# Kernel tuning notes

Hardware: AMD Instinct MI355X
Metric: run time of the kernel (lower is better)

The kernel has to match this reference:

```python
import jax, jax.numpy as jnp
import numpy as np

B, L, D = 4, 2048, 2048
H, KVH, HD = 16, 4, 128          # num_heads, num_kv_heads, head_dim = D // H
M = 16                           # mem_tokens
BASE = 10000.0
EPS = 1.1920929e-07              # torch F.rms_norm default eps = fp32 machine eps


def _rms_norm(x):
    # normalize over last dim, no learned weight (matches F.rms_norm(x, (hd,)))
    return x * jax.lax.rsqrt(jnp.mean(x * x, axis=-1, keepdims=True) + EPS)


def _apply_rotary(x, cos, sin):
    # x: [B, h, T, HD]; cos/sin: [1, 1, T, HD//2]
    half = x.shape[-1] // 2
    x1, x2 = x[..., :half], x[..., half:]
    return jnp.concatenate([x1 * cos + x2 * sin, -x1 * sin + x2 * cos], axis=-1)


def setup_inputs() -> dict:
    key = jax.random.key(0)
    k0, k1, k2, k3, k4 = jax.random.split(key, 5)
    kv_dim = KVH * HD
    s = 0.02
    return {
        "x": jax.random.normal(k0, (B, L, D), dtype=jnp.float32),
        "Wq": jax.random.normal(k1, (D, D), dtype=jnp.float32) * s,
        "Wk": jax.random.normal(k2, (kv_dim, D), dtype=jnp.float32) * s,
        "Wv": jax.random.normal(k3, (kv_dim, D), dtype=jnp.float32) * s,
        "Wproj": jax.random.normal(k4, (D, D), dtype=jnp.float32) * s,
        "q_gain": jnp.full((H,), 1.0, dtype=jnp.float32),
    }


def reference(x, Wq, Wk, Wv, Wproj, q_gain):
    Bx, Lx, Dx = x.shape
    # QKV projections (Linear: x @ W.T), split into heads -> [B, h, L, HD]
    q = (x @ Wq.T).reshape(Bx, Lx, H, HD).transpose(0, 2, 1, 3)
    k = (x @ Wk.T).reshape(Bx, Lx, KVH, HD).transpose(0, 2, 1, 3)
    v = (x @ Wv.T).reshape(Bx, Lx, KVH, HD).transpose(0, 2, 1, 3)
    # QK RMSNorm
    q = _rms_norm(q)
    k = _rms_norm(k)
    # RoPE on the non-memory tokens only
    T = Lx - M
    inv_freq = 1.0 / BASE ** (jnp.arange(0, HD, 2, dtype=jnp.float32) / HD)
    freqs = jnp.outer(jnp.arange(T, dtype=jnp.float32), inv_freq)  # [T, HD//2]
    cos = jnp.cos(freqs)[None, None]
    sin = jnp.sin(freqs)[None, None]
    q = jnp.concatenate([q[:, :, :M], _apply_rotary(q[:, :, M:], cos, sin)], axis=2)
    k = jnp.concatenate([k[:, :, :M], _apply_rotary(k[:, :, M:], cos, sin)], axis=2)
    # per-head gain on q
    q = q * q_gain[None, :, None, None]
    # GQA attention: group q heads by kv head (matches repeat_interleave ordering)
    rep = H // KVH
    qg = q.reshape(Bx, KVH, rep, Lx, HD)
    scale = 1.0 / np.sqrt(HD).astype(np.float32)
    scores = jnp.einsum('bgrqd,bgkd->bgrqk', qg, k) * scale  # [B, KVH, rep, L, L]
    causal = jnp.tril(jnp.ones((Lx, Lx), dtype=bool))
    scores = jnp.where(causal, scores, -jnp.inf)
    p = jax.nn.softmax(scores, axis=-1)
    y = jnp.einsum('bgrqk,bgkd->bgrqd', p, v)                # [B, KVH, rep, L, HD]
    y = y.reshape(Bx, H, Lx, HD).transpose(0, 2, 1, 3).reshape(Bx, Lx, Dx)
    return y @ Wproj.T
```

## Files before the change

### kernel.cpp

```cpp
#include <hip/hip_runtime.h>
#include <stdint.h>

typedef unsigned short u16;
typedef short s8v __attribute__((ext_vector_type(8)));
typedef float f4v __attribute__((ext_vector_type(4)));
typedef float f16v __attribute__((ext_vector_type(16)));

typedef __attribute__((address_space(1))) char gchar;
typedef __attribute__((address_space(3))) char lchar;

static __device__ __forceinline__ u16 f2bf(float f) {
  uint32_t x = __float_as_uint(f);
  x += 0x7fffu + ((x >> 16) & 1u);
  return (u16)(x >> 16);
}
static __device__ __forceinline__ float bf2f(u16 u) {
  return __uint_as_float(((uint32_t)u) << 16);
}
static __device__ __forceinline__ void gload_lds16(const void* g, void* l) {
  __builtin_amdgcn_global_load_lds((gchar*)(uintptr_t)g,
                                   (lchar*)(uint32_t)(uintptr_t)l, 16, 0, 0);
}

__global__ __launch_bounds__(256) void prep(const float4* __restrict__ x,
                                            const float4* __restrict__ wq,
                                            const float4* __restrict__ wk,
                                            const float4* __restrict__ wv,
                                            const float4* __restrict__ wp,
                                            uint2* __restrict__ xbf,
                                            uint2* __restrict__ wbf,
                                            float* __restrict__ tc,
                                            float* __restrict__ ts) {
  const int gid = blockIdx.x * 256 + threadIdx.x;
  const int st = gridDim.x * 256;
  for (int i = gid; i < 4194304; i += st) {
    float4 v = x[i];
    uint2 o;
    o.x = (uint32_t)f2bf(v.x) | ((uint32_t)f2bf(v.y) << 16);
    o.y = (uint32_t)f2bf(v.z) | ((uint32_t)f2bf(v.w) << 16);
    xbf[i] = o;
  }
  for (int i = gid; i < 2621440; i += st) {
    const float4* s;
    int off;
    if (i < 1048576)      { s = wq; off = i; }
    else if (i < 1310720) { s = wk; off = i - 1048576; }
    else if (i < 1572864) { s = wv; off = i - 1310720; }
    else                  { s = wp; off = i - 1572864; }
    float4 v = s[off];
    uint2 o;
    o.x = (uint32_t)f2bf(v.x) | ((uint32_t)f2bf(v.y) << 16);
    o.y = (uint32_t)f2bf(v.z) | ((uint32_t)f2bf(v.w) << 16);
    wbf[i] = o;
  }
  for (int i = gid; i < 2032 * 64; i += st) {
    int t = i >> 6, f = i & 63;
    float invf = 1.0f / powf(10000.0f, (float)f * (1.0f / 64.0f));
    float ang = (float)t * invf;
    float s, c;
    sincosf(ang, &s, &c);
    tc[i] = c;
    ts[i] = s;
  }
}

template <int OUT>
static __device__ __forceinline__ void gemm8_body(
    u16* sm, int bid, const u16* __restrict__ A, const u16* __restrict__ Wt,
    u16* __restrict__ Oa, float* __restrict__ OF) {
  const int tid = threadIdx.x;
  const int lane = tid & 63, wid = tid >> 6;
  const int wr = wid >> 2, wc = wid & 3;
  const int l15 = lane & 15, l4 = lane >> 4;

  const int swz = (bid & 7) * 32 + (bid >> 3);
  const int bm = swz >> 3, bn = swz & 7;
  const int m0 = bm * 256;
  const int n0r = bn * 256;

  auto pA = [&](int bs, int ks) { return sm + (bs * 2 + ks) * 8192; };
  auto pB = [&](int bs, int ks) { return sm + 32768 + (bs * 2 + ks) * 8192; };

  auto stage_part = [&](int kt, int bs, int ks) {
    const int kb = kt * 64 + ks * 32;
#pragma unroll
    for (int c = 0; c < 2; ++c) {
      int cidx = tid + c * 512;
      int r = cidx >> 2, q = cidx & 3;
      int cc = q ^ ((r >> 2) & 3);
      gload_lds16(A + (size_t)(m0 + r) * 2048 + kb + cc * 8,
                  pA(bs, ks) + cidx * 8);
    }
#pragma unroll
    for (int c = 0; c < 2; ++c) {
      int cidx = tid + c * 512;
      int r = cidx >> 2, q = cidx & 3;
      int cc = q ^ ((r >> 2) & 3);
      gload_lds16(Wt + (size_t)(n0r + r) * 2048 + kb + cc * 8,
                  pB(bs, ks) + cidx * 8);
    }
  };
  auto roff = [&](int fr, int c) {
    return (fr * 4 + (c ^ ((fr >> 2) & 3))) * 8;
  };

  const f4v Z4 = {0.f, 0.f, 0.f, 0.f};
  f4v acc[8][4];
#pragma unroll
  for (int i = 0; i < 8; i++)
#pragma unroll
    for (int j = 0; j < 4; j++) acc[i][j] = Z4;

  stage_part(0, 0, 0); stage_part(0, 0, 1);
  stage_part(1, 1, 0); stage_part(1, 1, 1);

  const int NT = 32;
  for (int t = 0; t < NT; ++t) {
    const int bs = t & 1;
    if (t + 1 < NT) asm volatile("s_waitcnt vmcnt(8)" ::: "memory");
    else            asm volatile("s_waitcnt vmcnt(0)" ::: "memory");
    asm volatile("s_barrier" ::: "memory");
    const bool pf = (t + 2 < NT);
#pragma unroll
    for (int ks = 0; ks < 2; ++ks) {
      s8v a[8], b[4];
#pragma unroll
      for (int i = 0; i < 8; ++i)
        a[i] = *(const s8v*)&pA(bs, ks)[roff(wr * 128 + i * 16 + l15, l4)];
#pragma unroll
      for (int j = 0; j < 4; ++j)
        b[j] = *(const s8v*)&pB(bs, ks)[roff(wc * 64 + j * 16 + l15, l4)];
      asm volatile("s_waitcnt lgkmcnt(0)" ::: "memory");
      __builtin_amdgcn_sched_barrier(0);
      asm volatile("s_barrier" ::: "memory");
      if (pf) stage_part(t + 2, bs, ks);
      __builtin_amdgcn_s_setprio(1);
#pragma unroll
      for (int i = 0; i < 8; ++i)
#pragma unroll
        for (int j = 0; j < 4; ++j)
          acc[i][j] = __builtin_amdgcn_mfma_f32_16x16x32_bf16(a[i], b[j], acc[i][j], 0, 0, 0);
      __builtin_amdgcn_s_setprio(0);
    }
  }

  const int colg = bn * 256 + wc * 64;
  if constexpr (OUT == 0) {
    const int hh = colg >> 7, d0 = colg & 127;
#pragma unroll
    for (int i = 0; i < 8; i++)
#pragma unroll
      for (int r = 0; r < 4; r++) {
        int m = m0 + wr * 128 + i * 16 + l4 * 4 + r;
        int b2 = m >> 11, l = m & 2047;
        size_t base = ((size_t)(b2 * 16 + hh) * 2048 + l) * 128 + d0;
#pragma unroll
        for (int j = 0; j < 4; j++)
          Oa[base + j * 16 + l15] = f2bf(acc[i][j][r]);
      }
  } else {
#pragma unroll
    for (int i = 0; i < 8; i++)
#pragma unroll
      for (int r = 0; r < 4; r++) {
        int m = m0 + wr * 128 + i * 16 + l4 * 4 + r;
#pragma unroll
        for (int j = 0; j < 4; j++)
          OF[(size_t)m * 2048 + colg + j * 16 + l15] = acc[i][j][r];
      }
  }
}

static __device__ __forceinline__ void gemm_kv_body(
    u16* sm, int bid, const u16* __restrict__ A, const u16* __restrict__ Wt,
    u16* __restrict__ Oa, u16* __restrict__ Ob2) {
  constexpr int MI = 4;
  const int tid = threadIdx.x;
  const int lane = tid & 63, wid = tid >> 6;
  const int wr = wid >> 1, wc = wid & 1;
  const int l15 = lane & 15, l4 = lane >> 4;

  const int swz = (bid & 7) * 32 + (bid >> 3);
  const int bm = swz >> 3, bn = swz & 7;
  const int m0 = bm * 256;
  const int n0r = bn * 128;

  auto pA = [&](int bs, int ks) { return sm + (bs * 2 + ks) * 8192; };
  auto pB = [&](int bs, int ks) { return sm + 32768 + (bs * 2 + ks) * 4096; };

  auto stage_part = [&](int kt, int bs, int ks) {
    const int kb = kt * 64 + ks * 32;
#pragma unroll
    for (int c = 0; c < 2; ++c) {
      int cidx = tid + c * 512;
      int r = cidx >> 2, q = cidx & 3;
      int cc = q ^ ((r >> 2) & 3);
      gload_lds16(A + (size_t)(m0 + r) * 2048 + kb + cc * 8,
                  pA(bs, ks) + cidx * 8);
    }
    {
      int cidx = tid;
      int r = cidx >> 2, q = cidx & 3;
      int cc = q ^ ((r >> 2) & 3);
      gload_lds16(Wt + (size_t)(n0r + r) * 2048 + kb + cc * 8,
                  pB(bs, ks) + cidx * 8);
    }
  };
  auto roff = [&](int fr, int c) {
    return (fr * 4 + (c ^ ((fr >> 2) & 3))) * 8;
  };

  const f4v Z4 = {0.f, 0.f, 0.f, 0.f};
  f4v acc[MI][4];
#pragma unroll
  for (int i = 0; i < MI; i++)
#pragma unroll
    for (int j = 0; j < 4; j++) acc[i][j] = Z4;

  stage_part(0, 0, 0); stage_part(0, 0, 1);
  stage_part(1, 1, 0); stage_part(1, 1, 1);

  const int NT = 32;
  for (int t = 0; t < NT; ++t) {
    const int bs = t & 1;
    if (t + 1 < NT) asm volatile("s_waitcnt vmcnt(6)" ::: "memory");
    else            asm volatile("s_waitcnt vmcnt(0)" ::: "memory");
    asm volatile("s_barrier" ::: "memory");
    const bool pf = (t + 2 < NT);
#pragma unroll
    for (int ks = 0; ks < 2; ++ks) {
      s8v afrg[MI], bfrg[4];
#pragma unroll
      for (int i = 0; i < MI; ++i)
        afrg[i] = *(const s8v*)&pA(bs, ks)[roff(wr * (MI * 16) + i * 16 + l15, l4)];
#pragma unroll
      for (int j = 0; j < 4; ++j)
        bfrg[j] = *(const s8v*)&pB(bs, ks)[roff(wc * 64 + j * 16 + l15, l4)];
      asm volatile("s_waitcnt lgkmcnt(0)" ::: "memory");
      __builtin_amdgcn_sched_barrier(0);
      asm volatile("s_barrier" ::: "memory");
      if (pf) stage_part(t + 2, bs, ks);
      __builtin_amdgcn_s_setprio(1);
#pragma unroll
      for (int i = 0; i < MI; ++i)
#pragma unroll
        for (int j = 0; j < 4; ++j)
          acc[i][j] = __builtin_amdgcn_mfma_f32_16x16x32_bf16(afrg[i], bfrg[j], acc[i][j], 0, 0, 0);
      __builtin_amdgcn_s_setprio(0);
    }
  }

  const int colg = bn * 128 + wc * 64;
  u16* Ob = (colg < 512) ? Oa : Ob2;
  const int hh = (colg & 511) >> 7, d0 = colg & 127;
#pragma unroll
  for (int i = 0; i < MI; i++)
#pragma unroll
    for (int r = 0; r < 4; r++) {
      int m = m0 + wr * (MI * 16) + i * 16 + l4 * 4 + r;
      int b = m >> 11, l = m & 2047;
      size_t base = ((size_t)(b * 4 + hh) * 2048 + l) * 128 + d0;
#pragma unroll
      for (int j = 0; j < 4; j++)
        Ob[base + j * 16 + l15] = f2bf(acc[i][j][r]);
    }
}

__global__ __launch_bounds__(512, 2) void gemm_qkv(
    const u16* __restrict__ x, const u16* __restrict__ wq,
    const u16* __restrict__ wkv, u16* __restrict__ q,
    u16* __restrict__ kO, u16* __restrict__ vO) {
  __shared__ u16 smem[65536];
  const int bid = (int)blockIdx.x;
  if (bid < 256) gemm8_body<0>(smem, bid, x, wq, q, nullptr);
  else           gemm_kv_body(smem, bid - 256, x, wkv, kO, vO);
}

__global__ __launch_bounds__(512, 2) void gemm_proj(
    const u16* __restrict__ y, const u16* __restrict__ wp, float* __restrict__ out) {
  __shared__ u16 smem[65536];
  gemm8_body<2>(smem, (int)blockIdx.x, y, wp, nullptr, out);
}

__global__ __launch_bounds__(256) void norm_transpose(
    u16* __restrict__ kbuf, const u16* __restrict__ v, u16* __restrict__ vt,
    const float* __restrict__ tc, const float* __restrict__ ts) {
  __shared__ u16 t[64][64];
  const int bid = (int)blockIdx.x;
  const int tid = threadIdx.x;
  if (bid < 1024) {
    const int l0 = (bid & 31) * 64, d0 = ((bid >> 5) & 1) * 64, bg = bid >> 6;
#pragma unroll
    for (int it = 0; it < 2; ++it) {
      int lin = it * 256 + tid;
      int r = lin >> 3, cb = lin & 7;
      s8v val = *(const s8v*)&v[((bg * 2048 + l0 + r) * 128) + d0 + cb * 8];
      *(s8v*)&t[r][(cb ^ (r & 7)) * 8] = val;
    }
    __syncthreads();
#pragma unroll
    for (int it = 0; it < 2; ++it) {
      int lin = it * 256 + tid;
      int r2 = lin >> 3, c2 = (lin & 7) * 8;
      s8v o;
#pragma unroll
      for (int j = 0; j < 8; ++j) {
        int rr = c2 + j, cc = r2;
        o[j] = (short)t[rr][(cc & 7) + 8 * ((cc >> 3) ^ (rr & 7))];
      }
      *(s8v*)&vt[((bg * 128 + d0 + r2) * 2048) + l0 + c2] = o;
    }
  } else {
    const int lane = tid & 63;
    const int gw = (bid - 1024) * 4 + (tid >> 6);
    for (int row = gw; row < 32768; row += 1024) {
      int l = row & 2047;
      u16* p = kbuf + (size_t)row * 128;
      float x1 = bf2f(p[lane]);
      float x2 = bf2f(p[lane + 64]);
      float ss = x1 * x1 + x2 * x2;
#pragma unroll
      for (int off = 32; off > 0; off >>= 1) ss += __shfl_xor(ss, off, 64);
      float r = rsqrtf(ss * (1.0f / 128.0f) + 1.1920929e-07f);
      x1 *= r; x2 *= r;
      if (l >= 16) {
        int tt = l - 16;
        float c = tc[tt * 64 + lane], s = ts[tt * 64 + lane];
        float o1 = x1 * c + x2 * s;
        float o2 = -x1 * s + x2 * c;
        x1 = o1; x2 = o2;
      }
      p[lane] = f2bf(x1);
      p[lane + 64] = f2bf(x2);
    }
  }
}

__global__ __launch_bounds__(512, 2) void attn(const u16* __restrict__ q,
                                               const u16* __restrict__ k,
                                               const u16* __restrict__ vt,
                                               u16* __restrict__ y,
                                               const float* __restrict__ qg,
                                               const float* __restrict__ tc,
                                               const float* __restrict__ ts) {
  __shared__ u16 lK[2][64 * 128];
  __shared__ u16 lVT[2][64 * 128];
  const int tid = threadIdx.x;
  const int lane = tid & 63, wid = tid >> 6;
  const int l31 = lane & 31, hi = lane >> 5;

  const int bid = (int)blockIdx.x;
  const int bg = (bid & 7) * 2 + (bid >> 7);
  const int pairi = (bid >> 3) & 15;
  const int b = bg >> 2, g = bg & 3;
  const int h = g * 4 + (wid & 3);
  const int se = wid >> 2;

  const u16* qh = q + (size_t)(b * 16 + h) * 2048 * 128;
  const u16* kb0 = k + (size_t)(b * 4 + g) * 2048 * 128;
  const u16* vtb0 = vt + (size_t)(b * 4 + g) * 128 * 2048;
  const float gscale = qg[h] * (0.08838834764831845f * 1.4426950408889634f);

  auto stage = [&](int t, int bufsel) {
    const int kv0 = t * 64;
#pragma unroll
    for (int it = 0; it < 2; ++it) {
      int lin = it * 512 + tid;
      int kj = lin >> 4, s = lin & 15;
      gload_lds16(kb0 + (size_t)(kv0 + kj) * 128 + ((s ^ (kj & 15)) * 8),
                  &lK[bufsel][lin * 8]);
    }
#pragma unroll
    for (int it = 0; it < 2; ++it) {
      int lin = it * 512 + tid;
      int r = lin >> 4, c = lin & 15;
      int gl = c ^ (r & 15);
      int d = 2 * r + (gl >> 3);
      gload_lds16(vtb0 + (size_t)d * 2048 + kv0 + ((gl & 7) * 8),
                  &lVT[bufsel][lin * 8]);
    }
  };

  for (int ph = 0; ph < 2; ++ph) {
    const int qt = ph ? (31 - pairi) : pairi;
    const int q0 = qt * 64;
    const int nt = qt + 1;
    const int pos = q0 + 32 * se + l31;

    s8v qf[8];
    {
      const u16* qp = qh + (size_t)pos * 128 + hi * 8;
      s8v qr[8];
#pragma unroll
      for (int ks = 0; ks < 8; ++ks) qr[ks] = *(const s8v*)&qp[ks * 16];
      float ssum = 0.f;
#pragma unroll
      for (int ks = 0; ks < 8; ++ks)
#pragma unroll
        for (int j = 0; j < 8; ++j) {
          float v = bf2f((u16)qr[ks][j]);
          ssum += v * v;
        }
      ssum += __shfl_xor(ssum, 32, 64);
      const float rn = rsqrtf(ssum * (1.0f / 128.0f) + 1.1920929e-07f) * gscale;
      const bool rot = (pos >= 16);
      const int tt = pos - 16;
#pragma unroll
      for (int ks = 0; ks < 4; ++ks) {
        float cv[8], sv[8];
        if (rot) {
          const float* cp = &tc[tt * 64 + ks * 16 + hi * 8];
          const float* sp = &ts[tt * 64 + ks * 16 + hi * 8];
          *(float4*)&cv[0] = *(const float4*)cp;
          *(float4*)&cv[4] = *(const float4*)(cp + 4);
          *(float4*)&sv[0] = *(const float4*)sp;
          *(float4*)&sv[4] = *(const float4*)(sp + 4);
        }
        uint32_t wlo[4], whi[4];
#pragma unroll
        for (int j2 = 0; j2 < 4; ++j2) {
          float o1[2], o2[2];
#pragma unroll
          for (int e = 0; e < 2; ++e) {
            const int j = j2 * 2 + e;
            float x1 = bf2f((u16)qr[ks][j]);
            float x2 = bf2f((u16)qr[ks + 4][j]);
            float a = x1, bb = x2;
            if (rot) { a = x1 * cv[j] + x2 * sv[j]; bb = x2 * cv[j] - x1 * sv[j]; }
            o1[e] = a * rn;
            o2[e] = bb * rn;
          }
          asm("v_cvt_pk_bf16_f32 %0, %1, %2" : "=v"(wlo[j2]) : "v"(o1[0]), "v"(o1[1]));
          asm("v_cvt_pk_bf16_f32 %0, %1, %2" : "=v"(whi[j2]) : "v"(o2[0]), "v"(o2[1]));
        }
        union { uint32_t u[4]; s8v v; } ua, ub;
        ua.u[0] = wlo[0]; ua.u[1] = wlo[1]; ua.u[2] = wlo[2]; ua.u[3] = wlo[3];
        ub.u[0] = whi[0]; ub.u[1] = whi[1]; ub.u[2] = whi[2]; ub.u[3] = whi[3];
        qf[ks] = ua.v;
        qf[ks + 4] = ub.v;
      }
    }

    f16v yacc[4];
#pragma unroll
    for (int j = 0; j < 4; ++j)
#pragma unroll
      for (int r = 0; r < 16; ++r) yacc[j][r] = 0.f;
    float mrow = -1e30f, lrow = 0.f;

    stage(0, 0);
    __syncthreads();

    for (int t = 0; t < nt; ++t) {
      const int cur = t & 1;
      if (t + 1 < nt) stage(t + 1, cur ^ 1);
      const int kv0 = t * 64;

      f16v s0a, s1a;
#pragma unroll
      for (int r = 0; r < 16; ++r) { s0a[r] = 0.f; s1a[r] = 0.f; }
      __builtin_amdgcn_s_setprio(1);
#pragma unroll
      for (int ks = 0; ks < 8; ++ks) {
        const int slot = (2 * ks + hi) ^ (l31 & 15);
        s8v kf0 = *(const s8v*)&lK[cur][(l31)*128 + slot * 8];
        s8v kf1 = *(const s8v*)&lK[cur][(32 + l31) * 128 + slot * 8];
        s0a = __builtin_amdgcn_mfma_f32_32x32x16_bf16(kf0, qf[ks], s0a, 0, 0, 0);
        s1a = __builtin_amdgcn_mfma_f32_32x32x16_bf16(kf1, qf[ks], s1a, 0, 0, 0);
      }
      __builtin_amdgcn_s_setprio(0);

      const bool last = (t == nt - 1);
      float p0[16], p1[16], mx[16];
#pragma unroll
      for (int r = 0; r < 16; ++r) {
        const int kvloc = (r & 3) + 8 * (r >> 2) + 4 * hi;
        float v0 = s0a[r];
        float v1 = s1a[r];
        if (last) {
          if (kv0 + kvloc > pos) v0 = -1e30f;
          if (kv0 + 32 + kvloc > pos) v1 = -1e30f;
        }
        p0[r] = v0; p1[r] = v1;
        mx[r] = fmaxf(v0, v1);
      }
#pragma unroll
      for (int s2 = 8; s2 > 0; s2 >>= 1)
#pragma unroll
        for (int r = 0; r < s2; ++r) mx[r] = fmaxf(mx[r], mx[r + s2]);
      float pmax = fmaxf(mx[0], __shfl_xor(mx[0], 32, 64));

      if (!__all(pmax - mrow <= 11.541560327111707f)) {
        float mnew = fmaxf(mrow, pmax);
        float corr = __builtin_amdgcn_exp2f(mrow - mnew);
#pragma unroll
        for (int r = 0; r < 16; ++r) {
          const int qloc = (r & 3) + 8 * (r >> 2) + 4 * hi;
          float cb = __shfl(corr, qloc, 64);
          yacc[0][r] *= cb; yacc[1][r] *= cb; yacc[2][r] *= cb; yacc[3][r] *= cb;
        }
        lrow *= corr;
        mrow = mnew;
      }

      float sm[16];
#pragma unroll
      for (int r = 0; r < 16; ++r) {
        float e0 = __builtin_amdgcn_exp2f(p0[r] - mrow);
        float e1 = __builtin_amdgcn_exp2f(p1[r] - mrow);
        p0[r] = e0; p1[r] = e1;
        sm[r] = e0 + e1;
      }
#pragma unroll
      for (int s2 = 8; s2 > 0; s2 >>= 1)
#pragma unroll
        for (int r = 0; r < s2; ++r) sm[r] += sm[r + s2];
      float ps = sm[0] + __shfl_xor(sm[0], 32, 64);
      lrow += ps;

      __builtin_amdgcn_s_setprio(1);
#pragma unroll
      for (int ks = 0; ks < 4; ++ks) {
        const float* pc = (ks < 2) ? p0 : p1;
        const int rb = 8 * (ks & 1);
        uint32_t A0, A1, B0, B1;
        asm("v_cvt_pk_bf16_f32 %0, %1, %2" : "=v"(A0) : "v"(pc[rb + 0]), "v"(pc[rb + 1]));
        asm("v_cvt_pk_bf16_f32 %0, %1, %2" : "=v"(A1) : "v"(pc[rb + 2]), "v"(pc[rb + 3]));
        asm("v_cvt_pk_bf16_f32 %0, %1, %2" : "=v"(B0) : "v"(pc[rb + 4]), "v"(pc[rb + 5]));
        asm("v_cvt_pk_bf16_f32 %0, %1, %2" : "=v"(B1) : "v"(pc[rb + 6]), "v"(pc[rb + 7]));
        asm("v_permlane32_swap_b32 %0, %1" : "+v"(A0), "+v"(B0));
        asm("v_permlane32_swap_b32 %0, %1" : "+v"(A1), "+v"(B1));
        union { uint32_t u[4]; s8v v; } uu;
        uu.u[0] = A0; uu.u[1] = A1; uu.u[2] = B0; uu.u[3] = B1;
#pragma unroll
        for (int jd = 0; jd < 4; ++jd) {
          const int rowd = 32 * jd + l31;
          const int line = rowd >> 1;
          const int gl = ((rowd & 1) << 3) | (2 * ks + hi);
          const int c = gl ^ (line & 15);
          s8v vf = *(const s8v*)&lVT[cur][line * 128 + c * 8];
          yacc[jd] = __builtin_amdgcn_mfma_f32_32x32x16_bf16(uu.v, vf, yacc[jd], 0, 0, 0);
        }
      }
      __builtin_amdgcn_s_setprio(0);
      __syncthreads();
    }

    float inv = 1.0f / lrow;
#pragma unroll
    for (int r = 0; r < 16; ++r) {
      const int qloc = (r & 3) + 8 * (r >> 2) + 4 * hi;
      float ib = __shfl(inv, qloc, 64);
      const int qrow = q0 + 32 * se + qloc;
      size_t base = ((size_t)(b * 2048 + qrow)) * 2048 + h * 128 + l31;
#pragma unroll
      for (int jd = 0; jd < 4; ++jd)
        y[base + 32 * jd] = f2bf(yacc[jd][r] * ib);
    }
  }
}

extern "C" void kernel_launch(void* const* d_in, const int* in_sizes, int n_in,
                              void* d_out, int out_size, void* d_ws, size_t ws_size,
                              hipStream_t stream) {
  const float* x  = (const float*)d_in[0];
  const float* Wq = (const float*)d_in[1];
  const float* Wk = (const float*)d_in[2];
  const float* Wv = (const float*)d_in[3];
  const float* Wp = (const float*)d_in[4];
  const float* qg = (const float*)d_in[5];
  float* out = (float*)d_out;

  char* ws = (char*)d_ws;
  size_t off = 0;
  auto alloc = [&](size_t bytes) {
    void* p = ws + off;
    off += (bytes + 255) & ~(size_t)255;
    return p;
  };
  u16* x_bf  = (u16*)alloc((size_t)8192 * 2048 * 2);
  u16* wq_bf = (u16*)alloc((size_t)2048 * 2048 * 2);
  u16* wk_bf = (u16*)alloc((size_t)512 * 2048 * 2);
  u16* wv_bf = (u16*)alloc((size_t)512 * 2048 * 2);
  u16* wp_bf = (u16*)alloc((size_t)2048 * 2048 * 2);
  u16* q_bf  = (u16*)alloc((size_t)4 * 16 * 2048 * 128 * 2);
  u16* k_bf  = (u16*)alloc((size_t)4 * 4 * 2048 * 128 * 2);
  u16* v_bf  = (u16*)alloc((size_t)4 * 4 * 2048 * 128 * 2);
  float* tab = (float*)alloc((size_t)2032 * 64 * 2 * 4);
  u16* y_bf  = x_bf;
  u16* vt_bf = wq_bf;
  (void)wv_bf;

  prep<<<2048, 256, 0, stream>>>((const float4*)x, (const float4*)Wq,
                                 (const float4*)Wk, (const float4*)Wv,
                                 (const float4*)Wp, (uint2*)x_bf, (uint2*)wq_bf,
                                 tab, tab + 2032 * 64);
  gemm_qkv<<<dim3(512), 512, 0, stream>>>(x_bf, wq_bf, wk_bf, q_bf, k_bf, v_bf);
  norm_transpose<<<dim3(1280), 256, 0, stream>>>(k_bf, v_bf, vt_bf,
                                                 tab, tab + 2032 * 64);
  attn<<<dim3(256), 512, 0, stream>>>(q_bf, k_bf, vt_bf, y_bf, qg,
                                      tab, tab + 2032 * 64);
  gemm_proj<<<dim3(256), 512, 0, stream>>>(y_bf, wp_bf, out);
}
```

Measured before the change: 324.8 us.

## Unify QKV/proj GEMMs into 256x128 tile kernel with single-stage prefetch

Replaces the 256x256 tile with 512 threads, and the separate KV body, by one templated GEMM body. It uses 256x128 tiles, 256 threads, a K-step of 32 and a double buffer prefetching one stage ahead. Grid counts double for proj and grow for QKV, and LDS per block drops to 48KB. The aim is better occupancy and load balance across CUs. In exchange each wave does less MFMA work per barrier, there are twice as many loop iterations and only one stage of prefetch depth, and operand reuse per tile is lower.

```diff
diff --git a/kernel.cpp b/kernel.cpp
--- a/kernel.cpp
+++ b/kernel.cpp
@@ -64,40 +64,39 @@
   }
 }
 
-template <int OUT>
-static __device__ __forceinline__ void gemm8_body(
+template <int NBN, int OUT>
+static __device__ __forceinline__ void gemm_body(
     u16* sm, int bid, const u16* __restrict__ A, const u16* __restrict__ Wt,
-    u16* __restrict__ Oa, float* __restrict__ OF) {
+    u16* __restrict__ Oa, u16* __restrict__ Ob2, float* __restrict__ OF) {
   const int tid = threadIdx.x;
   const int lane = tid & 63, wid = tid >> 6;
-  const int wr = wid >> 2, wc = wid & 3;
+  const int wr = wid >> 1, wc = wid & 1;
   const int l15 = lane & 15, l4 = lane >> 4;
 
-  const int swz = (bid & 7) * 32 + (bid >> 3);
-  const int bm = swz >> 3, bn = swz & 7;
+  const int nwg = 32 * NBN;
+  const int swz = (bid & 7) * (nwg >> 3) + (bid >> 3);
+  const int bm = swz / NBN, bn = swz % NBN;
   const int m0 = bm * 256;
-  const int n0r = bn * 256;
-
-  auto pA = [&](int bs, int ks) { return sm + (bs * 2 + ks) * 8192; };
-  auto pB = [&](int bs, int ks) { return sm + 32768 + (bs * 2 + ks) * 8192; };
-
-  auto stage_part = [&](int kt, int bs, int ks) {
-    const int kb = kt * 64 + ks * 32;
-#pragma unroll
-    for (int c = 0; c < 2; ++c) {
-      int cidx = tid + c * 512;
+  const int n0r = bn * 128;
+
+  auto pA = [&](int bs) { return sm + bs * 8192; };
+  auto pB = [&](int bs) { return sm + 16384 + bs * 4096; };
+
+  auto stage = [&](int kt, int bs) {
+    const int kb = kt * 32;
+#pragma unroll
+    for (int c = 0; c < 4; ++c) {
+      int cidx = tid + c * 256;
       int r = cidx >> 2, q = cidx & 3;
       int cc = q ^ ((r >> 2) & 3);
-      gload_lds16(A + (size_t)(m0 + r) * 2048 + kb + cc * 8,
-                  pA(bs, ks) + cidx * 8);
+      gload_lds16(A + (size_t)(m0 + r) * 2048 + kb + cc * 8, pA(bs) + cidx * 8);
     }
 #pragma unroll
     for (int c = 0; c < 2; ++c) {
-      int cidx = tid + c * 512;
+      int cidx = tid + c * 256;
       int r = cidx >> 2, q = cidx & 3;
       int cc = q ^ ((r >> 2) & 3);
-      gload_lds16(Wt + (size_t)(n0r + r) * 2048 + kb + cc * 8,
-                  pB(bs, ks) + cidx * 8);
+      gload_lds16(Wt + (size_t)(n0r + r) * 2048 + kb + cc * 8, pB(bs) + cidx * 8);
     }
   };
   auto roff = [&](int fr, int c) {
@@ -111,40 +110,39 @@
 #pragma unroll
     for (int j = 0; j < 4; j++) acc[i][j] = Z4;
 
-  stage_part(0, 0, 0); stage_part(0, 0, 1);
-  stage_part(1, 1, 0); stage_part(1, 1, 1);
-
-  const int NT = 32;
+  stage(0, 0);
+
+  const int NT = 64;
   for (int t = 0; t < NT; ++t) {
     const int bs = t & 1;
-    if (t + 1 < NT) asm volatile("s_waitcnt vmcnt(8)" ::: "memory");
-    else            asm volatile("s_waitcnt vmcnt(0)" ::: "memory");
+    asm volatile("s_waitcnt lgkmcnt(0)" ::: "memory");
+    __builtin_amdgcn_sched_barrier(0);
     asm volatile("s_barrier" ::: "memory");
-    const bool pf = (t + 2 < NT);
-#pragma unroll
-    for (int ks = 0; ks < 2; ++ks) {
-      s8v a[8], b[4];
-#pragma unroll
-      for (int i = 0; i < 8; ++i)
-        a[i] = *(const s8v*)&pA(bs, ks)[roff(wr * 128 + i * 16 + l15, l4)];
+    if (t + 1 < NT) {
+      stage(t + 1, bs ^ 1);
+      asm volatile("s_waitcnt vmcnt(6)" ::: "memory");
+    } else {
+      asm volatile("s_waitcnt vmcnt(0)" ::: "memory");
+    }
+    asm volatile("s_barrier" ::: "memory");
+
+    s8v a[8], b[4];
+#pragma unroll
+    for (int i = 0; i < 8; ++i)
+      a[i] = *(const s8v*)&pA(bs)[roff(wr * 128 + i * 16 + l15, l4)];
+#pragma unroll
+    for (int j = 0; j < 4; ++j)
+      b[j] = *(const s8v*)&pB(bs)[roff(wc * 64 + j * 16 + l15, l4)];
+    __builtin_amdgcn_s_setprio(1);
+#pragma unroll
+    for (int i = 0; i < 8; ++i)
 #pragma unroll
       for (int j = 0; j < 4; ++j)
-        b[j] = *(const s8v*)&pB(bs, ks)[roff(wc * 64 + j * 16 + l15, l4)];
-      asm volatile("s_waitcnt lgkmcnt(0)" ::: "memory");
-      __builtin_amdgcn_sched_barrier(0);
-      asm volatile("s_barrier" ::: "memory");
-      if (pf) stage_part(t + 2, bs, ks);
-      __builtin_amdgcn_s_setprio(1);
-#pragma unroll
-      for (int i = 0; i < 8; ++i)
-#pragma unroll
-        for (int j = 0; j < 4; ++j)
-          acc[i][j] = __builtin_amdgcn_mfma_f32_16x16x32_bf16(a[i], b[j], acc[i][j], 0, 0, 0);
-      __builtin_amdgcn_s_setprio(0);
-    }
-  }
-
-  const int colg = bn * 256 + wc * 64;
+        acc[i][j] = __builtin_amdgcn_mfma_f32_16x16x32_bf16(a[i], b[j], acc[i][j], 0, 0, 0);
+    __builtin_amdgcn_s_setprio(0);
+  }
+
+  const int colg = bn * 128 + wc * 64;
   if constexpr (OUT == 0) {
     const int hh = colg >> 7, d0 = colg & 127;
 #pragma unroll
@@ -158,12 +156,26 @@
         for (int j = 0; j < 4; j++)
           Oa[base + j * 16 + l15] = f2bf(acc[i][j][r]);
       }
-  } else {
+  } else if constexpr (OUT == 1) {
+    u16* Ob = (colg < 512) ? Oa : Ob2;
+    const int hh = (colg & 511) >> 7, d0 = colg & 127;
 #pragma unroll
     for (int i = 0; i < 8; i++)
 #pragma unroll
       for (int r = 0; r < 4; r++) {
         int m = m0 + wr * 128 + i * 16 + l4 * 4 + r;
+        int b2 = m >> 11, l = m & 2047;
+        size_t base = ((size_t)(b2 * 4 + hh) * 2048 + l) * 128 + d0;
+#pragma unroll
+        for (int j = 0; j < 4; j++)
+          Ob[base + j * 16 + l15] = f2bf(acc[i][j][r]);
+      }
+  } else {
+#pragma unroll
+    for (int i = 0; i < 8; i++)
+#pragma unroll
+      for (int r = 0; r < 4; r++) {
+        int m = m0 + wr * 128 + i * 16 + l4 * 4 + r;
 #pragma unroll
         for (int j = 0; j < 4; j++)
           OF[(size_t)m * 2048 + colg + j * 16 + l15] = acc[i][j][r];
@@ -171,115 +183,20 @@
   }
 }
 
-static __device__ __forceinline__ void gemm_kv_body(
-    u16* sm, int bid, const u16* __restrict__ A, const u16* __restrict__ Wt,
-    u16* __restrict__ Oa, u16* __restrict__ Ob2) {
-  constexpr int MI = 4;
-  const int tid = threadIdx.x;
-  const int lane = tid & 63, wid = tid >> 6;
-  const int wr = wid >> 1, wc = wid & 1;
-  const int l15 = lane & 15, l4 = lane >> 4;
-
-  const int swz = (bid & 7) * 32 + (bid >> 3);
-  const int bm = swz >> 3, bn = swz & 7;
-  const int m0 = bm * 256;
-  const int n0r = bn * 128;
-
-  auto pA = [&](int bs, int ks) { return sm + (bs * 2 + ks) * 8192; };
-  auto pB = [&](int bs, int ks) { return sm + 32768 + (bs * 2 + ks) * 4096; };
-
-  auto stage_part = [&](int kt, int bs, int ks) {
-    const int kb = kt * 64 + ks * 32;
-#pragma unroll
-    for (int c = 0; c < 2; ++c) {
-      int cidx = tid + c * 512;
-      int r = cidx >> 2, q = cidx & 3;
-      int cc = q ^ ((r >> 2) & 3);
-      gload_lds16(A + (size_t)(m0 + r) * 2048 + kb + cc * 8,
-                  pA(bs, ks) + cidx * 8);
-    }
-    {
-      int cidx = tid;
-      int r = cidx >> 2, q = cidx & 3;
-      int cc = q ^ ((r >> 2) & 3);
-      gload_lds16(Wt + (size_t)(n0r + r) * 2048 + kb + cc * 8,
-                  pB(bs, ks) + cidx * 8);
-    }
-  };
-  auto roff = [&](int fr, int c) {
-    return (fr * 4 + (c ^ ((fr >> 2) & 3))) * 8;
-  };
-
-  const f4v Z4 = {0.f, 0.f, 0.f, 0.f};
-  f4v acc[MI][4];
-#pragma unroll
-  for (int i = 0; i < MI; i++)
-#pragma unroll
-    for (int j = 0; j < 4; j++) acc[i][j] = Z4;
-
-  stage_part(0, 0, 0); stage_part(0, 0, 1);
-  stage_part(1, 1, 0); stage_part(1, 1, 1);
-
-  const int NT = 32;
-  for (int t = 0; t < NT; ++t) {
-    const int bs = t & 1;
-    if (t + 1 < NT) asm volatile("s_waitcnt vmcnt(6)" ::: "memory");
-    else            asm volatile("s_waitcnt vmcnt(0)" ::: "memory");
-    asm volatile("s_barrier" ::: "memory");
-    const bool pf = (t + 2 < NT);
-#pragma unroll
-    for (int ks = 0; ks < 2; ++ks) {
-      s8v afrg[MI], bfrg[4];
-#pragma unroll
-      for (int i = 0; i < MI; ++i)
-        afrg[i] = *(const s8v*)&pA(bs, ks)[roff(wr * (MI * 16) + i * 16 + l15, l4)];
-#pragma unroll
-      for (int j = 0; j < 4; ++j)
-        bfrg[j] = *(const s8v*)&pB(bs, ks)[roff(wc * 64 + j * 16 + l15, l4)];
-      asm volatile("s_waitcnt lgkmcnt(0)" ::: "memory");
-      __builtin_amdgcn_sched_barrier(0);
-      asm volatile("s_barrier" ::: "memory");
-      if (pf) stage_part(t + 2, bs, ks);
-      __builtin_amdgcn_s_setprio(1);
-#pragma unroll
-      for (int i = 0; i < MI; ++i)
-#pragma unroll
-        for (int j = 0; j < 4; ++j)
-          acc[i][j] = __builtin_amdgcn_mfma_f32_16x16x32_bf16(afrg[i], bfrg[j], acc[i][j], 0, 0, 0);
-      __builtin_amdgcn_s_setprio(0);
-    }
-  }
-
-  const int colg = bn * 128 + wc * 64;
-  u16* Ob = (colg < 512) ? Oa : Ob2;
-  const int hh = (colg & 511) >> 7, d0 = colg & 127;
-#pragma unroll
-  for (int i = 0; i < MI; i++)
-#pragma unroll
-    for (int r = 0; r < 4; r++) {
-      int m = m0 + wr * (MI * 16) + i * 16 + l4 * 4 + r;
-      int b = m >> 11, l = m & 2047;
-      size_t base = ((size_t)(b * 4 + hh) * 2048 + l) * 128 + d0;
-#pragma unroll
-      for (int j = 0; j < 4; j++)
-        Ob[base + j * 16 + l15] = f2bf(acc[i][j][r]);
-    }
-}
-
-__global__ __launch_bounds__(512, 2) void gemm_qkv(
+__global__ __launch_bounds__(256, 2) void gemm_qkv(
     const u16* __restrict__ x, const u16* __restrict__ wq,
     const u16* __restrict__ wkv, u16* __restrict__ q,
     u16* __restrict__ kO, u16* __restrict__ vO) {
-  __shared__ u16 smem[65536];
+  __shared__ u16 smem[24576];
   const int bid = (int)blockIdx.x;
-  if (bid < 256) gemm8_body<0>(smem, bid, x, wq, q, nullptr);
-  else           gemm_kv_body(smem, bid - 256, x, wkv, kO, vO);
-}
-
-__global__ __launch_bounds__(512, 2) void gemm_proj(
+  if (bid < 512) gemm_body<16, 0>(smem, bid, x, wq, q, nullptr, nullptr);
+  else           gemm_body<8, 1>(smem, bid - 512, x, wkv, kO, vO, nullptr);
+}
+
+__global__ __launch_bounds__(256, 2) void gemm_proj(
     const u16* __restrict__ y, const u16* __restrict__ wp, float* __restrict__ out) {
-  __shared__ u16 smem[65536];
-  gemm8_body<2>(smem, (int)blockIdx.x, y, wp, nullptr, out);
+  __shared__ u16 smem[24576];
+  gemm_body<16, 2>(smem, (int)blockIdx.x, y, wp, nullptr, nullptr, out);
 }
 
 __global__ __launch_bounds__(256) void norm_transpose(
@@ -595,10 +512,10 @@
                                  (const float4*)Wk, (const float4*)Wv,
                                  (const float4*)Wp, (uint2*)x_bf, (uint2*)wq_bf,
                                  tab, tab + 2032 * 64);
-  gemm_qkv<<<dim3(512), 512, 0, stream>>>(x_bf, wq_bf, wk_bf, q_bf, k_bf, v_bf);
+  gemm_qkv<<<dim3(768), 256, 0, stream>>>(x_bf, wq_bf, wk_bf, q_bf, k_bf, v_bf);
   norm_transpose<<<dim3(1280), 256, 0, stream>>>(k_bf, v_bf, vt_bf,
                                                  tab, tab + 2032 * 64);
   attn<<<dim3(256), 512, 0, stream>>>(q_bf, k_bf, vt_bf, y_bf, qg,
                                       tab, tab + 2032 * 64);
-  gemm_proj<<<dim3(256), 512, 0, stream>>>(y_bf, wp_bf, out);
-}
+  gemm_proj<<<dim3(512), 256, 0, stream>>>(y_bf, wp_bf, out);
+}
```

Result: no change. 330.9 us (+1.9%).
